# Performance work log

Hardware: AMD Instinct MI355X
Metric: run time of the kernel (lower is better)

The kernel has to match this reference:

```python
import jax, jax.numpy as jnp
import numpy as np

H, W = 96, 96
THRESHOLD = 0.9
C = 256

def setup_inputs() -> dict:
    key = jax.random.key(0)
    k1, k2 = jax.random.split(key)
    return {
        "feature_query": jax.random.normal(k1, (C, H, W), jnp.float32),
        "feature_projection": jax.random.normal(k2, (C, H, W), jnp.float32),
    }

def reference(feature_query, feature_projection):
    c = feature_query.shape[0]
    # flatten spatial dims -> [C, N]; L2-normalize each pixel's descriptor over channels
    q = feature_query.reshape(c, -1)
    p = feature_projection.reshape(c, -1)
    q = q / jnp.linalg.norm(q, axis=0, keepdims=True)
    p = p / jnp.linalg.norm(p, axis=0, keepdims=True)
    # cosine similarity matrix [N, M] (GEMM)
    sim = jnp.einsum('cn,cm->nm', q, p)
    col_max = jnp.argmax(sim, axis=0)   # [M] best query row per projection column
    row_max = jnp.argmax(sim, axis=1)   # [N] best projection column per query row
    j = jnp.arange(sim.shape[1])
    q_idx = col_max                      # candidate query index for each column j
    sim_vals = sim[q_idx, j]
    # mutual nearest-neighbor + threshold (fixed-shape boolean mask instead of
    # a data-dependent python list, for jit compatibility)
    mutual = (row_max[q_idx] == j) & (sim_vals > THRESHOLD)
    # oneDim2TwoDim: (idx // W, idx % W), valid only if div+1 < H
    q_div, q_mod = q_idx // W, q_idx % W
    p_div, p_mod = j // W, j % W
    valid = mutual & (q_div + 1 < H) & (p_div + 1 < H)
    return sim, valid, q_idx, q_div, q_mod, p_div, p_mod
```

## Files before the change

### kernel.cpp

```cpp
#include <hip/hip_runtime.h>
#include <hip/hip_fp16.h>

#define N_PIX 9216
#define CCH 256
#define W_ 96
#define H_ 96
#define BM 128
#define BN 128
#define BK 16
#define TM 8
#define TN 8

typedef _Float16 half8_t __attribute__((ext_vector_type(8)));
typedef float f32x4_t __attribute__((ext_vector_type(4)));

__device__ __forceinline__ unsigned int mono_enc(float f) {
    unsigned int u = __float_as_uint(f);
    return (u & 0x80000000u) ? ~u : (u | 0x80000000u);
}
__device__ __forceinline__ float mono_dec(unsigned int e) {
    return __uint_as_float((e & 0x80000000u) ? (e ^ 0x80000000u) : ~e);
}


__global__ __launch_bounds__(256) void norms_kernel(const float* __restrict__ Q,
                                                    const float* __restrict__ P,
                                                    float* __restrict__ invq,
                                                    float* __restrict__ invp) {
    int n = blockIdx.x * blockDim.x + threadIdx.x;
    if (n >= N_PIX) return;
    float sq = 0.f, sp = 0.f;
    for (int c = 0; c < CCH; ++c) {
        float a = Q[(size_t)c * N_PIX + n];
        float b = P[(size_t)c * N_PIX + n];
        sq = fmaf(a, a, sq);
        sp = fmaf(b, b, sp);
    }
    invq[n] = 1.0f / sqrtf(sq);
    invp[n] = 1.0f / sqrtf(sp);
}

__device__ __forceinline__ int local_row(int ty, int i) {
    return (i < 4) ? (ty * 4 + i) : (64 + ty * 4 + (i - 4));
}
__device__ __forceinline__ int local_col(int tx, int j) {
    return (j < 4) ? (tx * 4 + j) : (64 + tx * 4 + (j - 4));
}

__global__ __launch_bounds__(256) void gemm_kernel(const float* __restrict__ Q,
                                                   const float* __restrict__ P,
                                                   const float* __restrict__ invq,
                                                   const float* __restrict__ invp,
                                                   float* __restrict__ sim,
                                                   unsigned long long* __restrict__ row_best,
                                                   unsigned long long* __restrict__ col_best) {
    __shared__ union SH {
        struct { float A[BK][BM]; float B[BK][BN]; } t;
        unsigned long long red[16][128];
    } sh;

    const int tid = threadIdx.x;
    const int tx = tid & 15;
    const int ty = tid >> 4;
    const int n0 = blockIdx.y * BM;
    const int m0 = blockIdx.x * BN;

    float acc[TM][TN];
#pragma unroll
    for (int i = 0; i < TM; ++i)
#pragma unroll
        for (int j = 0; j < TN; ++j) acc[i][j] = 0.f;

    for (int kk = 0; kk < CCH; kk += BK) {
#pragma unroll
        for (int rep = 0; rep < 2; ++rep) {
            int idx = tid + rep * 256;
            int row = idx >> 5;
            int c4  = idx & 31;
            float4 av = *(const float4*)&Q[(size_t)(kk + row) * N_PIX + n0 + c4 * 4];
            float4 bv = *(const float4*)&P[(size_t)(kk + row) * N_PIX + m0 + c4 * 4];
            *(float4*)&sh.t.A[row][c4 * 4] = av;
            *(float4*)&sh.t.B[row][c4 * 4] = bv;
        }
        __syncthreads();
#pragma unroll
        for (int k = 0; k < BK; ++k) {
            float a[TM], b[TN];
            *(float4*)&a[0] = *(const float4*)&sh.t.A[k][ty * 4];
            *(float4*)&a[4] = *(const float4*)&sh.t.A[k][ty * 4 + 64];
            *(float4*)&b[0] = *(const float4*)&sh.t.B[k][tx * 4];
            *(float4*)&b[4] = *(const float4*)&sh.t.B[k][tx * 4 + 64];
#pragma unroll
            for (int i = 0; i < TM; ++i)
#pragma unroll
                for (int j = 0; j < TN; ++j)
                    acc[i][j] = fmaf(a[i], b[j], acc[i][j]);
        }
        __syncthreads();
    }

    float iq[TM], ip[TN];
#pragma unroll
    for (int i = 0; i < TM; ++i) iq[i] = invq[n0 + local_row(ty, i)];
#pragma unroll
    for (int j = 0; j < TN; ++j) ip[j] = invp[m0 + local_col(tx, j)];
#pragma unroll
    for (int i = 0; i < TM; ++i)
#pragma unroll
        for (int j = 0; j < TN; ++j) acc[i][j] *= iq[i] * ip[j];

#pragma unroll
    for (int i = 0; i < TM; ++i) {
        int n = n0 + local_row(ty, i);
        float4 v0 = make_float4(acc[i][0], acc[i][1], acc[i][2], acc[i][3]);
        float4 v1 = make_float4(acc[i][4], acc[i][5], acc[i][6], acc[i][7]);
        float* dst = &sim[(size_t)n * N_PIX + m0];
        *(float4*)(dst + tx * 4) = v0;
        *(float4*)(dst + 64 + tx * 4) = v1;
    }

#pragma unroll
    for (int i = 0; i < TM; ++i) {
        float best = acc[i][0]; int bj = 0;
#pragma unroll
        for (int j = 1; j < TN; ++j)
            if (acc[i][j] > best) { best = acc[i][j]; bj = j; }
        unsigned int gcol = (unsigned int)(m0 + local_col(tx, bj));
        sh.red[tx][local_row(ty, i)] =
            ((unsigned long long)mono_enc(best) << 32) | (unsigned long long)(0xFFFFFFFFu - gcol);
    }
    __syncthreads();
    if (tid < 128) {
        unsigned long long best = sh.red[0][tid];
#pragma unroll
        for (int x = 1; x < 16; ++x) {
            unsigned long long v = sh.red[x][tid];
            if (v > best) best = v;
        }
        atomicMax(&row_best[n0 + tid], best);
    }
    __syncthreads();

#pragma unroll
    for (int j = 0; j < TN; ++j) {
        float best = acc[0][j]; int bi = 0;
#pragma unroll
        for (int i = 1; i < TM; ++i)
            if (acc[i][j] > best) { best = acc[i][j]; bi = i; }
        unsigned int grow = (unsigned int)(n0 + local_row(ty, bi));
        sh.red[ty][local_col(tx, j)] =
            ((unsigned long long)mono_enc(best) << 32) | (unsigned long long)(0xFFFFFFFFu - grow);
    }
    __syncthreads();
    if (tid < 128) {
        unsigned long long best = sh.red[0][tid];
#pragma unroll
        for (int x = 1; x < 16; ++x) {
            unsigned long long v = sh.red[x][tid];
            if (v > best) best = v;
        }
        atomicMax(&col_best[m0 + tid], best);
    }
}


__device__ __forceinline__ unsigned int pack_pair(float x, float y, float& rx, float& ry) {
    __half hx = __float2half(x), hy = __float2half(y);
    rx = x - __half2float(hx);
    ry = y - __half2float(hy);
    return (unsigned int)__half_as_ushort(hx) | ((unsigned int)__half_as_ushort(hy) << 16);
}

__global__ __launch_bounds__(256) void prep_kernel(const float* __restrict__ Q,
                                                   const float* __restrict__ P,
                                                   uint4* __restrict__ qh,
                                                   uint4* __restrict__ ql,
                                                   uint4* __restrict__ ph,
                                                   uint4* __restrict__ pl,
                                                   float* __restrict__ invq,
                                                   float* __restrict__ invp) {
    __shared__ float rq[4][64];
    __shared__ float rp[4][64];
    const int lane = threadIdx.x & 63;
    const int band = threadIdx.x >> 6;
    const int n = blockIdx.x * 64 + lane;
    float sq = 0.f, sp = 0.f;
    for (int kb = band * 8; kb < band * 8 + 8; ++kb) {
        float a[8], b[8];
#pragma unroll
        for (int t = 0; t < 8; ++t) {
            a[t] = Q[(size_t)(kb * 8 + t) * N_PIX + n];
            b[t] = P[(size_t)(kb * 8 + t) * N_PIX + n];
        }
#pragma unroll
        for (int t = 0; t < 8; ++t) {
            sq = fmaf(a[t], a[t], sq);
            sp = fmaf(b[t], b[t], sp);
        }
        uint4 vqh, vql, vph, vpl;
        unsigned int* uqh = (unsigned int*)&vqh;
        unsigned int* uql = (unsigned int*)&vql;
        unsigned int* uph = (unsigned int*)&vph;
        unsigned int* upl = (unsigned int*)&vpl;
#pragma unroll
        for (int j = 0; j < 4; ++j) {
            float r0, r1;
            uqh[j] = pack_pair(a[2 * j], a[2 * j + 1], r0, r1);
            uql[j] = (unsigned int)__half_as_ushort(__float2half(r0))
                   | ((unsigned int)__half_as_ushort(__float2half(r1)) << 16);
            uph[j] = pack_pair(b[2 * j], b[2 * j + 1], r0, r1);
            upl[j] = (unsigned int)__half_as_ushort(__float2half(r0))
                   | ((unsigned int)__half_as_ushort(__float2half(r1)) << 16);
        }
        size_t o = (size_t)kb * N_PIX + n;
        qh[o] = vqh; ql[o] = vql; ph[o] = vph; pl[o] = vpl;
    }
    rq[band][lane] = sq;
    rp[band][lane] = sp;
    __syncthreads();
    if (threadIdx.x < 64) {
        float tq = rq[0][lane] + rq[1][lane] + rq[2][lane] + rq[3][lane];
        float tp = rp[0][lane] + rp[1][lane] + rp[2][lane] + rp[3][lane];
        invq[n] = 1.0f / sqrtf(tq);
        invp[n] = 1.0f / sqrtf(tp);
    }
}

__global__ __launch_bounds__(256, 3) void mfma_gemm_kernel(
        const uint4* __restrict__ QH, const uint4* __restrict__ QL,
        const uint4* __restrict__ PH, const uint4* __restrict__ PL,
        const float* __restrict__ invq, const float* __restrict__ invp,
        float* __restrict__ sim,
        unsigned long long* __restrict__ row_best,
        unsigned long long* __restrict__ col_best) {
    const unsigned int bid = blockIdx.x;
    const unsigned int xcd = bid & 7u;
    const unsigned int nbl = bid >> 3;
    const unsigned int gg  = nbl / 72u;
    const unsigned int rr  = nbl % 72u;
    const unsigned int by  = xcd * 9u + (rr >> 3);
    const unsigned int bx  = gg * 8u + (rr & 7u);

    const int tid = threadIdx.x;
    const int l  = tid & 63;
    const int w  = tid >> 6;
    const int rl = l & 15;
    const int kg = l >> 4;
    const int r0 = (int)by * 128 + (w >> 1) * 64;
    const int c0 = (int)bx * 128 + (w & 1) * 64;

    __shared__ float st[4][16][68];

    const f32x4_t zero4 = {0.f, 0.f, 0.f, 0.f};
    f32x4_t acc[4][4];
#pragma unroll
    for (int i = 0; i < 4; ++i)
#pragma unroll
        for (int j = 0; j < 4; ++j) acc[i][j] = zero4;

    const int rA = r0 + rl;
    const int cB = c0 + rl;

    const uint4* pqh = QH + (size_t)kg * N_PIX + rA;
    const uint4* pql = QL + (size_t)kg * N_PIX + rA;
    const uint4* pph = PH + (size_t)kg * N_PIX + cB;
    const uint4* ppl = PL + (size_t)kg * N_PIX + cB;

#pragma unroll 2
    for (int ks = 0; ks < 8; ++ks) {
        half8_t ah[4], al4[4], bh4[4], bl4[4];
#pragma unroll
        for (int f = 0; f < 4; ++f) {
            ah[f]  = *(const half8_t*)(pqh + f * 16);
            al4[f] = *(const half8_t*)(pql + f * 16);
            bh4[f] = *(const half8_t*)(pph + f * 16);
            bl4[f] = *(const half8_t*)(ppl + f * 16);
        }
        pqh += 4 * N_PIX; pql += 4 * N_PIX; pph += 4 * N_PIX; ppl += 4 * N_PIX;
#pragma unroll
        for (int fr = 0; fr < 4; ++fr)
#pragma unroll
            for (int fc = 0; fc < 4; ++fc) {
                acc[fr][fc] = __builtin_amdgcn_mfma_f32_16x16x32_f16(ah[fr],  bh4[fc], acc[fr][fc], 0, 0, 0);
                acc[fr][fc] = __builtin_amdgcn_mfma_f32_16x16x32_f16(ah[fr],  bl4[fc], acc[fr][fc], 0, 0, 0);
                acc[fr][fc] = __builtin_amdgcn_mfma_f32_16x16x32_f16(al4[fr], bh4[fc], acc[fr][fc], 0, 0, 0);
            }
    }

    float iq[4][4];
#pragma unroll
    for (int fr = 0; fr < 4; ++fr) {
        const float4 v = *(const float4*)&invq[r0 + fr * 16 + kg * 4];
        iq[fr][0] = v.x; iq[fr][1] = v.y; iq[fr][2] = v.z; iq[fr][3] = v.w;
    }
    float ip[4];
#pragma unroll
    for (int fc = 0; fc < 4; ++fc) ip[fc] = invp[c0 + fc * 16 + rl];

#pragma unroll
    for (int fr = 0; fr < 4; ++fr)
#pragma unroll
        for (int fc = 0; fc < 4; ++fc)
#pragma unroll
            for (int j = 0; j < 4; ++j)
                acc[fr][fc][j] *= iq[fr][j] * ip[fc];

#pragma unroll
    for (int fr = 0; fr < 4; ++fr)
#pragma unroll
        for (int j = 0; j < 4; ++j) {
            float best = acc[fr][0][j];
            int bf = 0;
#pragma unroll
            for (int fc = 1; fc < 4; ++fc)
                if (acc[fr][fc][j] > best) { best = acc[fr][fc][j]; bf = fc; }
            const unsigned int gcol = (unsigned int)(c0 + bf * 16 + rl);
            unsigned long long key = ((unsigned long long)mono_enc(best) << 32)
                                   | (unsigned long long)(0xFFFFFFFFu - gcol);
#pragma unroll
            for (int m = 1; m < 16; m <<= 1) {
                unsigned long long o = __shfl_xor(key, m, 64);
                if (o > key) key = o;
            }
            if (rl == 0)
                atomicMax(&row_best[r0 + fr * 16 + kg * 4 + j], key);
        }

#pragma unroll
    for (int fc = 0; fc < 4; ++fc) {
        float best = acc[0][fc][0];
        unsigned int brow = (unsigned int)(r0 + kg * 4);
#pragma unroll
        for (int fr = 0; fr < 4; ++fr)
#pragma unroll
            for (int j = 0; j < 4; ++j) {
                float v = acc[fr][fc][j];
                unsigned int rr2 = (unsigned int)(r0 + fr * 16 + kg * 4 + j);
                if (v > best) { best = v; brow = rr2; }
            }
        unsigned long long key = ((unsigned long long)mono_enc(best) << 32)
                               | (unsigned long long)(0xFFFFFFFFu - brow);
#pragma unroll
        for (int m = 16; m < 64; m <<= 1) {
            unsigned long long o = __shfl_xor(key, m, 64);
            if (o > key) key = o;
        }
        if (kg == 0)
            atomicMax(&col_best[c0 + fc * 16 + rl], key);
    }

#pragma unroll
    for (int fr = 0; fr < 4; ++fr) {
        asm volatile("s_waitcnt lgkmcnt(0)" ::: "memory");
#pragma unroll
        for (int fc = 0; fc < 4; ++fc)
#pragma unroll
            for (int j = 0; j < 4; ++j)
                st[w][kg * 4 + j][fc * 16 + rl] = acc[fr][fc][j];
        asm volatile("s_waitcnt lgkmcnt(0)" ::: "memory");
#pragma unroll
        for (int pass = 0; pass < 4; ++pass) {
            const int rowL = pass * 4 + kg;
            const f32x4_t v = *(const f32x4_t*)&st[w][rowL][rl * 4];
            const int gr = r0 + fr * 16 + rowL;
            __builtin_nontemporal_store(v, (f32x4_t*)(sim + (size_t)gr * N_PIX + c0 + rl * 4));
        }
    }
}


__global__ __launch_bounds__(256) void epilogue_kernel(const unsigned long long* __restrict__ row_best,
                                                       const unsigned long long* __restrict__ col_best,
                                                       float* __restrict__ out) {
    int j = blockIdx.x * blockDim.x + threadIdx.x;
    if (j >= N_PIX) return;
    unsigned long long cb = col_best[j];
    unsigned int q_idx = 0xFFFFFFFFu - (unsigned int)(cb & 0xFFFFFFFFull);
    float simval = mono_dec((unsigned int)(cb >> 32));
    unsigned long long rb = row_best[q_idx];
    unsigned int rm = 0xFFFFFFFFu - (unsigned int)(rb & 0xFFFFFFFFull);
    bool mutual = (rm == (unsigned int)j) && (simval > 0.9f);
    int qd = (int)(q_idx / W_), qm = (int)(q_idx % W_);
    int pd = j / W_, pm = j % W_;
    bool valid = mutual && (qd + 1 < H_) && (pd + 1 < H_);
    size_t base = (size_t)N_PIX * N_PIX;
    out[base + 0 * (size_t)N_PIX + j] = valid ? 1.0f : 0.0f;
    out[base + 1 * (size_t)N_PIX + j] = (float)q_idx;
    out[base + 2 * (size_t)N_PIX + j] = (float)qd;
    out[base + 3 * (size_t)N_PIX + j] = (float)qm;
    out[base + 4 * (size_t)N_PIX + j] = (float)pd;
    out[base + 5 * (size_t)N_PIX + j] = (float)pm;
}

extern "C" void kernel_launch(void* const* d_in, const int* in_sizes, int n_in,
                              void* d_out, int out_size, void* d_ws, size_t ws_size,
                              hipStream_t stream) {
    const float* Q = (const float*)d_in[0];
    const float* P = (const float*)d_in[1];
    float* out = (float*)d_out;

    unsigned long long* row_best = (unsigned long long*)d_ws;
    unsigned long long* col_best = row_best + N_PIX;
    float* invq = (float*)(col_best + N_PIX);
    float* invp = invq + N_PIX;

    hipMemsetAsync(d_ws, 0, 2 * N_PIX * sizeof(unsigned long long), stream);

    const size_t base_bytes = 2 * N_PIX * sizeof(unsigned long long) + 2 * N_PIX * sizeof(float);
    const size_t arr_u4 = (size_t)(CCH / 8) * N_PIX;
    const size_t need = base_bytes + 4 * arr_u4 * sizeof(uint4);

    if (ws_size >= need) {
        uint4* qh = (uint4*)((char*)d_ws + base_bytes);
        uint4* ql = qh + arr_u4;
        uint4* ph = ql + arr_u4;
        uint4* pl = ph + arr_u4;

        prep_kernel<<<N_PIX / 64, 256, 0, stream>>>(Q, P, qh, ql, ph, pl, invq, invp);
        mfma_gemm_kernel<<<5184, 256, 0, stream>>>(qh, ql, ph, pl, invq, invp,
                                                   out, row_best, col_best);
    } else {
        norms_kernel<<<N_PIX / 256, 256, 0, stream>>>(Q, P, invq, invp);
        dim3 grid(N_PIX / BN, N_PIX / BM);
        gemm_kernel<<<grid, 256, 0, stream>>>(Q, P, invq, invp, out, row_best, col_best);
    }

    epilogue_kernel<<<N_PIX / 256, 256, 0, stream>>>(row_best, col_best, out);
}
```

Measured before the change: 485.2 us.

## Stage GEMM operand tiles in LDS with double-buffered direct global-to-LDS loads

Before this change each wave loaded its A/B fragments straight from global memory, so a block's waves fetched the same tiles more than once. Now each wave loads one of the four operand planes (Q-hi, Q-lo, P-hi, P-lo) for the whole 128x128 block into LDS using global_load_lds. The LDS is double-buffered so the next K-step's fetch overlaps the current MFMAs. The staging buffer shares space with the epilogue transpose buffer through a union, and the occupancy hint drops from 3 to 2 blocks per CU. This adds a barrier every K-step and lowers occupancy. The GEMM is short (K=256) and the kernel is likely bound by writing the sim matrix, so the gain may be limited.

```diff
diff --git a/kernel.cpp b/kernel.cpp
--- a/kernel.cpp
+++ b/kernel.cpp
@@ -20,6 +20,12 @@
 }
 __device__ __forceinline__ float mono_dec(unsigned int e) {
     return __uint_as_float((e & 0x80000000u) ? (e ^ 0x80000000u) : ~e);
+}
+
+__device__ __forceinline__ void gload_lds16(const uint4* g, uint4* lds) {
+    __builtin_amdgcn_global_load_lds(
+        (const __attribute__((address_space(1))) unsigned int*)g,
+        (__attribute__((address_space(3))) unsigned int*)lds, 16, 0, 0);
 }
 
 
@@ -226,7 +232,7 @@
     }
 }
 
-__global__ __launch_bounds__(256, 3) void mfma_gemm_kernel(
+__global__ __launch_bounds__(256, 2) void mfma_gemm_kernel(
         const uint4* __restrict__ QH, const uint4* __restrict__ QL,
         const uint4* __restrict__ PH, const uint4* __restrict__ PL,
         const float* __restrict__ invq, const float* __restrict__ invp,
@@ -246,10 +252,15 @@
     const int w  = tid >> 6;
     const int rl = l & 15;
     const int kg = l >> 4;
-    const int r0 = (int)by * 128 + (w >> 1) * 64;
-    const int c0 = (int)bx * 128 + (w & 1) * 64;
-
-    __shared__ float st[4][16][68];
+    const int n0 = (int)by * 128;
+    const int m0 = (int)bx * 128;
+    const int r0 = n0 + (w >> 1) * 64;
+    const int c0 = m0 + (w & 1) * 64;
+
+    __shared__ union SH2 {
+        uint4 stage[2][4][4][128];
+        float st[4][16][68];
+    } sh;
 
     const f32x4_t zero4 = {0.f, 0.f, 0.f, 0.f};
     f32x4_t acc[4][4];
@@ -258,25 +269,40 @@
 #pragma unroll
         for (int j = 0; j < 4; ++j) acc[i][j] = zero4;
 
-    const int rA = r0 + rl;
-    const int cB = c0 + rl;
-
-    const uint4* pqh = QH + (size_t)kg * N_PIX + rA;
-    const uint4* pql = QL + (size_t)kg * N_PIX + rA;
-    const uint4* pph = PH + (size_t)kg * N_PIX + cB;
-    const uint4* ppl = PL + (size_t)kg * N_PIX + cB;
-
-#pragma unroll 2
-    for (int ks = 0; ks < 8; ++ks) {
+    const uint4* gsrc = (w == 0) ? (QH + n0) : (w == 1) ? (QL + n0)
+                      : (w == 2) ? (PH + m0) : (PL + m0);
+
+#pragma unroll
+    for (int kb = 0; kb < 4; ++kb)
+#pragma unroll
+        for (int h = 0; h < 2; ++h)
+            gload_lds16(gsrc + (size_t)kb * N_PIX + h * 64 + l,
+                        &sh.stage[0][w][kb][h * 64]);
+    asm volatile("s_waitcnt vmcnt(0)" ::: "memory");
+    __syncthreads();
+
+    const int ar = (w >> 1) * 64 + rl;
+    const int br = (w & 1) * 64 + rl;
+
+    for (int s = 0; s < 8; ++s) {
+        const int cur = s & 1;
+        if (s < 7) {
+            const uint4* gs = gsrc + (size_t)((s + 1) * 4) * N_PIX;
+#pragma unroll
+            for (int kb = 0; kb < 4; ++kb)
+#pragma unroll
+                for (int h = 0; h < 2; ++h)
+                    gload_lds16(gs + (size_t)kb * N_PIX + h * 64 + l,
+                                &sh.stage[cur ^ 1][w][kb][h * 64]);
+        }
         half8_t ah[4], al4[4], bh4[4], bl4[4];
 #pragma unroll
         for (int f = 0; f < 4; ++f) {
-            ah[f]  = *(const half8_t*)(pqh + f * 16);
-            al4[f] = *(const half8_t*)(pql + f * 16);
-            bh4[f] = *(const half8_t*)(pph + f * 16);
-            bl4[f] = *(const half8_t*)(ppl + f * 16);
-        }
-        pqh += 4 * N_PIX; pql += 4 * N_PIX; pph += 4 * N_PIX; ppl += 4 * N_PIX;
+            ah[f]  = *(const half8_t*)&sh.stage[cur][0][kg][ar + f * 16];
+            al4[f] = *(const half8_t*)&sh.stage[cur][1][kg][ar + f * 16];
+            bh4[f] = *(const half8_t*)&sh.stage[cur][2][kg][br + f * 16];
+            bl4[f] = *(const half8_t*)&sh.stage[cur][3][kg][br + f * 16];
+        }
 #pragma unroll
         for (int fr = 0; fr < 4; ++fr)
 #pragma unroll
@@ -285,6 +311,8 @@
                 acc[fr][fc] = __builtin_amdgcn_mfma_f32_16x16x32_f16(ah[fr],  bl4[fc], acc[fr][fc], 0, 0, 0);
                 acc[fr][fc] = __builtin_amdgcn_mfma_f32_16x16x32_f16(al4[fr], bh4[fc], acc[fr][fc], 0, 0, 0);
             }
+        asm volatile("s_waitcnt vmcnt(0)" ::: "memory");
+        __syncthreads();
     }
 
     float iq[4][4];
@@ -356,12 +384,12 @@
         for (int fc = 0; fc < 4; ++fc)
 #pragma unroll
             for (int j = 0; j < 4; ++j)
-                st[w][kg * 4 + j][fc * 16 + rl] = acc[fr][fc][j];
+                sh.st[w][kg * 4 + j][fc * 16 + rl] = acc[fr][fc][j];
         asm volatile("s_waitcnt lgkmcnt(0)" ::: "memory");
 #pragma unroll
         for (int pass = 0; pass < 4; ++pass) {
             const int rowL = pass * 4 + kg;
-            const f32x4_t v = *(const f32x4_t*)&st[w][rowL][rl * 4];
+            const f32x4_t v = *(const f32x4_t*)&sh.st[w][rowL][rl * 4];
             const int gr = r0 + fr * 16 + rowL;
             __builtin_nontemporal_store(v, (f32x4_t*)(sim + (size_t)gr * N_PIX + c0 + rl * 4));
         }
```

After: 467.9 us. -3.6%, faster.
